# Optimization experiments

Hardware: AMD Instinct MI355X
Metric: run time of the kernel (lower is better)

Reference implementation:

```python
import jax, jax.numpy as jnp
import numpy as np

B, N, D, C = 2, 65536, 128, 128          # batch, n_entries, input_dim, channel_dim
DEG, N_ACTIVE, STRIDE = 16, 4096, 16     # ring-neighbor sparse structure


def _build_indices():
    """Replicates the original module's Python intersection loops exactly,
    flattening them into (src_i, src_j, pair_out) gather/scatter index arrays.
    k[:, e, :] = sum_m a[:, i_th[m], :] * b[:, j_th[m], :] for each write slot e.
    Each slot e is written exactly once, so scatter-add == the original set."""
    neigh = [[] for _ in range(N)]
    for t in range(N_ACTIVE):
        i = t * STRIDE
        neigh[i] = [((t + dlt) % N_ACTIVE) * STRIDE for dlt in range(1, DEG + 1)]
    src_i, src_j, out = [], [], []
    e = 0
    for i in range(N):
        if not neigh[i]:
            continue
        i_element = list(neigh[i]) + [i]
        i_set = set(i_element)
        for j in neigh[i]:
            j_list = neigh[j]
            j_set = set(j_list)
            j_th = [m for m in j_list if m in i_set]      # order of j's list
            i_th = [m for m in i_element if m in j_set]   # order of i_element
            for ai, bi in zip(i_th, j_th):
                src_i.append(ai)
                src_j.append(bi)
                out.append(e)
            e += 1
    return (np.asarray(src_i, np.int32), np.asarray(src_j, np.int32),
            np.asarray(out, np.int32))


def setup_inputs() -> dict:
    key = jax.random.key(0)
    ks = jax.random.split(key, 8)
    s = 1.0 / np.sqrt(D)
    src_i, src_j, pair_out = _build_indices()
    return {
        "x": jax.random.normal(ks[0], (B, N, D), jnp.float32),
        "ln_in_w": jnp.ones((D,), jnp.float32),
        "ln_in_b": jnp.zeros((D,), jnp.float32),
        "Wla": jax.random.normal(ks[1], (C, D), jnp.float32) * s,
        "bla": jnp.zeros((C,), jnp.float32),
        "Wga": jax.random.normal(ks[2], (C, D), jnp.float32) * s,
        "bga": jnp.zeros((C,), jnp.float32),
        "Wlb": jax.random.normal(ks[3], (C, D), jnp.float32) * s,
        "blb": jnp.zeros((C,), jnp.float32),
        "Wgb": jax.random.normal(ks[4], (C, D), jnp.float32) * s,
        "bgb": jnp.zeros((C,), jnp.float32),
        "ln_o_w": jnp.ones((C,), jnp.float32),
        "ln_o_b": jnp.zeros((C,), jnp.float32),
        "Wgo": jax.random.normal(ks[5], (D, D), jnp.float32) * s,
        "bgo": jnp.zeros((D,), jnp.float32),
        "Wlo": jax.random.normal(ks[6], (D, C), jnp.float32) * s,
        "blo": jnp.zeros((D,), jnp.float32),
        "src_i": jnp.asarray(src_i),
        "src_j": jnp.asarray(src_j),
        "pair_out": jnp.asarray(pair_out),
    }


def _layernorm(x, w, b, eps=1e-5):
    mu = jnp.mean(x, axis=-1, keepdims=True)
    var = jnp.mean(jnp.square(x - mu), axis=-1, keepdims=True)
    return (x - mu) * jax.lax.rsqrt(var + eps) * w + b


def reference(x, ln_in_w, ln_in_b, Wla, bla, Wga, bga, Wlb, blb, Wgb, bgb,
              ln_o_w, ln_o_b, Wgo, bgo, Wlo, blo, src_i, src_j, pair_out):
    xn = _layernorm(x, ln_in_w, ln_in_b)                              # [B,N,D]
    a = jax.nn.sigmoid(xn @ Wga.T + bga) * (xn @ Wla.T + bla)         # [B,N,C]
    b = jax.nn.sigmoid(xn @ Wgb.T + bgb) * (xn @ Wlb.T + blb)         # [B,N,C]
    # triangular update: gather-multiply-sum-scatter over precomputed pairs
    prod = a[:, src_i, :] * b[:, src_j, :]                            # [B,P,C]
    k = jnp.zeros_like(a).at[:, pair_out, :].add(prod)                # [B,N,C]
    out = jax.nn.sigmoid(xn @ Wgo.T + bgo) * (_layernorm(k, ln_o_w, ln_o_b) @ Wlo.T + blo)
    return out
```

## Files before the change

kernel.cpp:

```cpp
#include <hip/hip_runtime.h>


#define BB 2
#define NN 65536
#define DD 128
#define CC 128
#define NA 4096
#define STR 16
#define WSZ 16384

typedef short short4v __attribute__((ext_vector_type(4)));
typedef short short8v __attribute__((ext_vector_type(8)));
typedef __bf16 bf16x8 __attribute__((ext_vector_type(8)));
typedef float f32x4 __attribute__((ext_vector_type(4)));
typedef float f32x2 __attribute__((ext_vector_type(2)));

__device__ __forceinline__ float sigf(float v) { return 1.0f / (1.0f + __expf(-v)); }
__device__ __forceinline__ short nbf(float f) {
    union { __bf16 h; short s; } u; u.h = (__bf16)f; return u.s;
}
__device__ __forceinline__ float bf2f(short b) {
    union { unsigned u; float f; } v; v.u = ((unsigned)(unsigned short)b) << 16;
    return v.f;
}
__device__ __forceinline__ bf16x8 s2b(short8v s) {
    union { short8v s; bf16x8 b; } u; u.s = s; return u.b;
}

__global__ __launch_bounds__(256)
void kern_wcvt(const float* __restrict__ Wla, const float* __restrict__ Wga,
               const float* __restrict__ Wlb, const float* __restrict__ Wgb,
               const float* __restrict__ Wgo, const float* __restrict__ Wlo,
               const float* __restrict__ lnw, const float* __restrict__ lnb,
               const float* __restrict__ lnow, const float* __restrict__ lnob,
               const float* __restrict__ bla, const float* __restrict__ bga,
               const float* __restrict__ blb, const float* __restrict__ bgb,
               const float* __restrict__ bgo, const float* __restrict__ blo,
               short* __restrict__ wbf, float* __restrict__ vtab)
{
    const int b = blockIdx.x;
    if (b < 64) {
        const int i  = b * 256 + threadIdx.x;
        const int ch = i >> 7, d = i & 127;
        const int pos = ((ch >> 4) * 4 + (d >> 5)) * 512
                      + ((((d >> 3) & 3) * 16 + (ch & 15)) * 8) + (d & 7);
        const float wi = lnw[d], wo = lnow[d];
        wbf[pos]           = nbf(Wla[i] * wi);
        wbf[WSZ + pos]     = nbf(Wga[i] * wi);
        wbf[2 * WSZ + pos] = nbf(Wlb[i] * wi);
        wbf[3 * WSZ + pos] = nbf(Wgb[i] * wi);
        wbf[4 * WSZ + pos] = nbf(Wgo[i] * wi);
        wbf[5 * WSZ + pos] = nbf(Wlo[i] * wo);
    } else {
        const int t = (b - 64) * 256 + threadIdx.x;
        const int m = t >> 7, c = t & 127;
        const float* Wr = (m == 0) ? Wla : (m == 1) ? Wga : (m == 2) ? Wlb
                        : (m == 3) ? Wgb : (m == 4) ? Wgo : Wlo;
        const float* bb = (m == 5) ? lnob : lnb;
        const float* ww = (m == 5) ? lnow : lnw;
        const float* bi = (m == 0) ? bla : (m == 1) ? bga : (m == 2) ? blb
                        : (m == 3) ? bgb : (m == 4) ? bgo : blo;
        const float* row = Wr + (size_t)c * DD;
        float av = 0.f, as = 0.f;
        for (int d = 0; d < DD; d += 4) {
            const f32x4 w4 = *(const f32x4*)(row + d);
            const f32x4 b4 = *(const f32x4*)(bb + d);
            const f32x4 g4 = *(const f32x4*)(ww + d);
            av += w4[0]*b4[0] + w4[1]*b4[1] + w4[2]*b4[2] + w4[3]*b4[3];
            as += w4[0]*g4[0] + w4[1]*g4[1] + w4[2]*g4[2] + w4[3]*g4[3];
        }
        vtab[m * 128 + c]       = av + bi[c];
        vtab[768 + m * 128 + c] = as;
    }
}

__global__ __launch_bounds__(256)
void kern_ab(const float* __restrict__ x, const short* __restrict__ wbf,
             const float* __restrict__ vtab, float* __restrict__ cbuf)
{
    const int wv    = threadIdx.x >> 6;
    const int l     = threadIdx.x & 63;
    const int bid   = blockIdx.x * 4 + wv;
    const int batch = bid >> 9;
    const int t0    = ((bid & 511) >> 1) << 4;
    const int nt0   = (bid & 1) * 4;
    const int lr    = l & 15;
    const int q     = l >> 4;
    const int fl    = l * 8;

    const float* xr = x + ((size_t)batch * NN + (size_t)(t0 + lr) * STR) * DD + q * 8;
    f32x4 v[4][2];
    #pragma unroll
    for (int kk = 0; kk < 4; ++kk) {
        v[kk][0] = *(const f32x4*)(xr + kk * 32);
        v[kk][1] = *(const f32x4*)(xr + kk * 32 + 4);
    }
    float s = 0.f, ss = 0.f;
    #pragma unroll
    for (int kk = 0; kk < 4; ++kk)
        #pragma unroll
        for (int h = 0; h < 2; ++h)
            #pragma unroll
            for (int j = 0; j < 4; ++j) { const float f = v[kk][h][j]; s += f; ss += f * f; }
    s += __shfl_xor(s, 16); ss += __shfl_xor(ss, 16);
    s += __shfl_xor(s, 32); ss += __shfl_xor(ss, 32);
    const float mu = s * (1.0f / 128.0f);
    const float rs = rsqrtf(ss * (1.0f / 128.0f) - mu * mu + 1e-5f);
    const float p  = -mu * rs;

    bf16x8 af[4];
    #pragma unroll
    for (int kk = 0; kk < 4; ++kk) {
        short8v t;
        #pragma unroll
        for (int j = 0; j < 4; ++j) {
            t[j]     = nbf(v[kk][0][j] * rs + p);
            t[4 + j] = nbf(v[kk][1][j] * rs + p);
        }
        af[kk] = s2b(t);
    }

    const short* wla = wbf;
    const short* wga = wbf + WSZ;
    const short* wlb = wbf + 2 * WSZ;
    const short* wgb = wbf + 3 * WSZ;

    #pragma unroll
    for (int nt = 0; nt < 4; ++nt) {
        const int col  = (nt0 + nt) * 16 + lr;
        const int base = ((nt0 + nt) * 4) * 512 + fl;
        f32x4 ala = {0.f,0.f,0.f,0.f}, aga = {0.f,0.f,0.f,0.f};
        f32x4 alb = {0.f,0.f,0.f,0.f}, agb = {0.f,0.f,0.f,0.f};
        #pragma unroll
        for (int kk = 0; kk < 4; ++kk) {
            const int o = base + kk * 512;
            ala = __builtin_amdgcn_mfma_f32_16x16x32_bf16(af[kk], *(const bf16x8*)(wla + o), ala, 0, 0, 0);
            aga = __builtin_amdgcn_mfma_f32_16x16x32_bf16(af[kk], *(const bf16x8*)(wga + o), aga, 0, 0, 0);
            alb = __builtin_amdgcn_mfma_f32_16x16x32_bf16(af[kk], *(const bf16x8*)(wlb + o), alb, 0, 0, 0);
            agb = __builtin_amdgcn_mfma_f32_16x16x32_bf16(af[kk], *(const bf16x8*)(wgb + o), agb, 0, 0, 0);
        }
        const float vla = vtab[col], vga = vtab[128 + col];
        const float vlb = vtab[256 + col], vgb = vtab[384 + col];
        #pragma unroll
        for (int r = 0; r < 4; ++r) {
            const float av = sigf(aga[r] + vga) * (ala[r] + vla);
            const float bv = sigf(agb[r] + vgb) * (alb[r] + vlb);
            cbuf[((size_t)batch * NA + t0 + q * 4 + r) * CC + col] = av * bv;
        }
    }
}

__global__ __launch_bounds__(64)
void kern_out(const float* __restrict__ x, const short* __restrict__ wbf,
              const float* __restrict__ vtab, const float* __restrict__ cbuf,
              float* __restrict__ out)
{
    __shared__ short kls[2][16][136];
    __shared__ float kst[2][16][2];
    const int bid   = blockIdx.x;
    const int swz   = (bid & 7) * 512 + (bid >> 3);
    const int batch = swz >> 11;
    const int ib    = swz & 2047;
    const int row0  = ib * 32;
    const int t0    = ib * 2;

    const int l  = threadIdx.x;
    const int lr = l & 15, lk = l >> 4;
    const int fl = l * 8;

    f32x4 v[2][4][2];
    #pragma unroll
    for (int g = 0; g < 2; ++g) {
        const float* xr = x + ((size_t)batch * NN + row0 + g * 16 + lr) * DD + lk * 8;
        #pragma unroll
        for (int kk = 0; kk < 4; ++kk) {
            v[g][kk][0] = *(const f32x4*)(xr + kk * 32);
            v[g][kk][1] = *(const f32x4*)(xr + kk * 32 + 4);
        }
    }

    const int sg = l >> 5;
    const int c4 = (l & 31) * 4;
    const int t  = t0 + sg;
    f32x4 cv[15];
    #pragma unroll
    for (int sx = 14; sx >= 0; --sx)
        cv[sx] = *(const f32x4*)(cbuf + ((size_t)batch * NA + ((t + sx + 2) & (NA - 1))) * CC + c4);

    {
        short4v z = {0, 0, 0, 0};
        *(short4v*)&kls[sg][15][c4] = z;
        float s0 = 0.f, s1 = 0.f, s2 = 0.f, s3 = 0.f;
        #pragma unroll
        for (int sx = 14; sx >= 0; --sx) {
            s0 += cv[sx][0]; s1 += cv[sx][1]; s2 += cv[sx][2]; s3 += cv[sx][3];
            short4v o; o[0] = nbf(s0); o[1] = nbf(s1); o[2] = nbf(s2); o[3] = nbf(s3);
            *(short4v*)&kls[sg][sx][c4] = o;
        }
    }

    bf16x8 afx[2][4];
    #pragma unroll
    for (int g = 0; g < 2; ++g) {
        float s = 0.f, ss = 0.f;
        #pragma unroll
        for (int kk = 0; kk < 4; ++kk)
            #pragma unroll
            for (int h = 0; h < 2; ++h)
                #pragma unroll
                for (int j = 0; j < 4; ++j) { const float f = v[g][kk][h][j]; s += f; ss += f * f; }
        s += __shfl_xor(s, 16); ss += __shfl_xor(ss, 16);
        s += __shfl_xor(s, 32); ss += __shfl_xor(ss, 32);
        const float mu = s * (1.0f / 128.0f);
        const float rs = rsqrtf(ss * (1.0f / 128.0f) - mu * mu + 1e-5f);
        const float p  = -mu * rs;
        #pragma unroll
        for (int kk = 0; kk < 4; ++kk) {
            short8v o;
            #pragma unroll
            for (int j = 0; j < 4; ++j) {
                o[j]     = nbf(v[g][kk][0][j] * rs + p);
                o[4 + j] = nbf(v[g][kk][1][j] * rs + p);
            }
            afx[g][kk] = s2b(o);
        }
    }

    bf16x8 afk[2][4];
    short8v kraw[2][4];
    #pragma unroll
    for (int g = 0; g < 2; ++g)
        #pragma unroll
        for (int kk = 0; kk < 4; ++kk) {
            kraw[g][kk] = *(const short8v*)&kls[g][lr][kk * 32 + lk * 8];
            afk[g][kk]  = s2b(kraw[g][kk]);
        }

    #pragma unroll
    for (int g = 0; g < 2; ++g) {
        float ks = 0.f, kss = 0.f;
        #pragma unroll
        for (int kk = 0; kk < 4; ++kk)
            #pragma unroll
            for (int j = 0; j < 8; ++j) { const float f = bf2f(kraw[g][kk][j]); ks += f; kss += f * f; }
        ks += __shfl_xor(ks, 16); kss += __shfl_xor(kss, 16);
        ks += __shfl_xor(ks, 32); kss += __shfl_xor(kss, 32);
        const float kmu = ks * (1.0f / 128.0f);
        const float krs = rsqrtf(kss * (1.0f / 128.0f) - kmu * kmu + 1e-5f);
        if (lk == 0) { kst[g][lr][0] = krs; kst[g][lr][1] = -kmu * krs; }
    }
    f32x2 kp[2][4];
    #pragma unroll
    for (int g = 0; g < 2; ++g)
        #pragma unroll
        for (int r = 0; r < 4; ++r)
            kp[g][r] = *(const f32x2*)&kst[g][lk * 4 + r][0];

    const short* wgo = wbf + 4 * WSZ;
    const short* wlo = wbf + 5 * WSZ;
    const float* vgo = vtab + 4 * 128;
    const float* vlo = vtab + 5 * 128;
    const float* slo = vtab + 768 + 5 * 128;
    #pragma unroll
    for (int nt = 0; nt < 8; ++nt) {
        bf16x8 bg_[4], bh_[4];
        #pragma unroll
        for (int kk = 0; kk < 4; ++kk) {
            bg_[kk] = *(const bf16x8*)(wgo + (nt * 4 + kk) * 512 + fl);
            bh_[kk] = *(const bf16x8*)(wlo + (nt * 4 + kk) * 512 + fl);
        }
        f32x4 ag0 = {0.f,0.f,0.f,0.f}, ag1 = {0.f,0.f,0.f,0.f};
        f32x4 ah0 = {0.f,0.f,0.f,0.f}, ah1 = {0.f,0.f,0.f,0.f};
        #pragma unroll
        for (int kk = 0; kk < 4; ++kk) {
            ag0 = __builtin_amdgcn_mfma_f32_16x16x32_bf16(afx[0][kk], bg_[kk], ag0, 0, 0, 0);
            ag1 = __builtin_amdgcn_mfma_f32_16x16x32_bf16(afx[1][kk], bg_[kk], ag1, 0, 0, 0);
            ah0 = __builtin_amdgcn_mfma_f32_16x16x32_bf16(afk[0][kk], bh_[kk], ah0, 0, 0, 0);
            ah1 = __builtin_amdgcn_mfma_f32_16x16x32_bf16(afk[1][kk], bh_[kk], ah1, 0, 0, 0);
        }
        const int   col = nt * 16 + lr;
        const float vg  = vgo[col];
        const float vl  = vlo[col];
        const float sl  = slo[col];
        #pragma unroll
        for (int r = 0; r < 4; ++r) {
            const size_t rowa = (size_t)batch * NN + row0 + lk * 4 + r;
            const float h0 = kp[0][r][0] * ah0[r] + (kp[0][r][1] * sl + vl);
            const float h1 = kp[1][r][0] * ah1[r] + (kp[1][r][1] * sl + vl);
            out[rowa * DD + col]        = sigf(ag0[r] + vg) * h0;
            out[(rowa + 16) * DD + col] = sigf(ag1[r] + vg) * h1;
        }
    }
}

extern "C" void kernel_launch(void* const* d_in, const int* in_sizes, int n_in,
                              void* d_out, int out_size, void* d_ws, size_t ws_size,
                              hipStream_t stream)
{
    const float* x    = (const float*)d_in[0];
    const float* lnw  = (const float*)d_in[1];
    const float* lnb  = (const float*)d_in[2];
    const float* Wla  = (const float*)d_in[3];
    const float* bla  = (const float*)d_in[4];
    const float* Wga  = (const float*)d_in[5];
    const float* bga  = (const float*)d_in[6];
    const float* Wlb  = (const float*)d_in[7];
    const float* blb  = (const float*)d_in[8];
    const float* Wgb  = (const float*)d_in[9];
    const float* bgb  = (const float*)d_in[10];
    const float* lnow = (const float*)d_in[11];
    const float* lnob = (const float*)d_in[12];
    const float* Wgo  = (const float*)d_in[13];
    const float* bgo  = (const float*)d_in[14];
    const float* Wlo  = (const float*)d_in[15];
    const float* blo  = (const float*)d_in[16];

    float* cbuf = (float*)d_ws;
    short* wbf  = (short*)((char*)d_ws + (size_t)BB * NA * CC * 4);
    float* vtab = (float*)((char*)wbf + 6 * WSZ * sizeof(short));
    float* out  = (float*)d_out;

    hipLaunchKernelGGL(kern_wcvt, dim3(67), dim3(256), 0, stream,
                       Wla, Wga, Wlb, Wgb, Wgo, Wlo,
                       lnw, lnb, lnow, lnob,
                       bla, bga, blb, bgb, bgo, blo, wbf, vtab);
    hipLaunchKernelGGL(kern_ab, dim3(BB * 128), dim3(256), 0, stream,
                       x, wbf, vtab, cbuf);
    hipLaunchKernelGGL(kern_out, dim3(BB * 2048), dim3(64), 0, stream,
                       x, wbf, vtab, cbuf, out);
}
```

Measured before the change: 56.67 us.

## Switch output projection to 32x32x16 MFMA with matching weight layout

Rewrites the output kernel to use 32x32x16 bf16 MFMA instead of pairs of 16x16x32 MFMAs. The Wgo/Wlo weights are repacked into a 32-column tile layout, and the x and k fragments are reloaded in the matching lane mapping. This reduces the number of MFMA issues and per-tile weight loads. The cost is a new 16-row output scatter pattern and larger accumulator register use.

After: 59.46 us. 4.9% more time.

```diff
diff --git a/kernel.cpp b/kernel.cpp
--- a/kernel.cpp
+++ b/kernel.cpp
@@ -14,6 +14,7 @@
 typedef __bf16 bf16x8 __attribute__((ext_vector_type(8)));
 typedef float f32x4 __attribute__((ext_vector_type(4)));
 typedef float f32x2 __attribute__((ext_vector_type(2)));
+typedef float f32x16 __attribute__((ext_vector_type(16)));
 
 __device__ __forceinline__ float sigf(float v) { return 1.0f / (1.0f + __expf(-v)); }
 __device__ __forceinline__ short nbf(float f) {
@@ -42,15 +43,17 @@
     if (b < 64) {
         const int i  = b * 256 + threadIdx.x;
         const int ch = i >> 7, d = i & 127;
-        const int pos = ((ch >> 4) * 4 + (d >> 5)) * 512
-                      + ((((d >> 3) & 3) * 16 + (ch & 15)) * 8) + (d & 7);
+        const int pos16 = ((ch >> 4) * 4 + (d >> 5)) * 512
+                        + ((((d >> 3) & 3) * 16 + (ch & 15)) * 8) + (d & 7);
+        const int pos32 = ((ch >> 5) * 8 + (d >> 4)) * 512
+                        + ((((d >> 3) & 1) * 32 + (ch & 31)) * 8) + (d & 7);
         const float wi = lnw[d], wo = lnow[d];
-        wbf[pos]           = nbf(Wla[i] * wi);
-        wbf[WSZ + pos]     = nbf(Wga[i] * wi);
-        wbf[2 * WSZ + pos] = nbf(Wlb[i] * wi);
-        wbf[3 * WSZ + pos] = nbf(Wgb[i] * wi);
-        wbf[4 * WSZ + pos] = nbf(Wgo[i] * wi);
-        wbf[5 * WSZ + pos] = nbf(Wlo[i] * wo);
+        wbf[pos16]           = nbf(Wla[i] * wi);
+        wbf[WSZ + pos16]     = nbf(Wga[i] * wi);
+        wbf[2 * WSZ + pos16] = nbf(Wlb[i] * wi);
+        wbf[3 * WSZ + pos16] = nbf(Wgb[i] * wi);
+        wbf[4 * WSZ + pos32] = nbf(Wgo[i] * wi);
+        wbf[5 * WSZ + pos32] = nbf(Wlo[i] * wo);
     } else {
         const int t = (b - 64) * 256 + threadIdx.x;
         const int m = t >> 7, c = t & 127;
@@ -156,7 +159,7 @@
               float* __restrict__ out)
 {
     __shared__ short kls[2][16][136];
-    __shared__ float kst[2][16][2];
+    __shared__ float kst[32][2];
     const int bid   = blockIdx.x;
     const int swz   = (bid & 7) * 512 + (bid >> 3);
     const int batch = swz >> 11;
@@ -164,24 +167,13 @@
     const int row0  = ib * 32;
     const int t0    = ib * 2;
 
-    const int l  = threadIdx.x;
-    const int lr = l & 15, lk = l >> 4;
-    const int fl = l * 8;
-
-    f32x4 v[2][4][2];
-    #pragma unroll
-    for (int g = 0; g < 2; ++g) {
-        const float* xr = x + ((size_t)batch * NN + row0 + g * 16 + lr) * DD + lk * 8;
-        #pragma unroll
-        for (int kk = 0; kk < 4; ++kk) {
-            v[g][kk][0] = *(const f32x4*)(xr + kk * 32);
-            v[g][kk][1] = *(const f32x4*)(xr + kk * 32 + 4);
-        }
-    }
-
-    const int sg = l >> 5;
-    const int c4 = (l & 31) * 4;
-    const int t  = t0 + sg;
+    const int l   = threadIdx.x;
+    const int idx = l & 31;
+    const int q   = l >> 5;
+    const int fl  = l * 8;
+
+    const int c4 = idx * 4;
+    const int t  = t0 + q;
     f32x4 cv[15];
     #pragma unroll
     for (int sx = 14; sx >= 0; --sx)
@@ -189,72 +181,70 @@
 
     {
         short4v z = {0, 0, 0, 0};
-        *(short4v*)&kls[sg][15][c4] = z;
+        *(short4v*)&kls[q][15][c4] = z;
         float s0 = 0.f, s1 = 0.f, s2 = 0.f, s3 = 0.f;
         #pragma unroll
         for (int sx = 14; sx >= 0; --sx) {
             s0 += cv[sx][0]; s1 += cv[sx][1]; s2 += cv[sx][2]; s3 += cv[sx][3];
             short4v o; o[0] = nbf(s0); o[1] = nbf(s1); o[2] = nbf(s2); o[3] = nbf(s3);
-            *(short4v*)&kls[sg][sx][c4] = o;
-        }
-    }
-
-    bf16x8 afx[2][4];
-    #pragma unroll
-    for (int g = 0; g < 2; ++g) {
+            *(short4v*)&kls[q][sx][c4] = o;
+        }
+    }
+
+    const float* xr = x + ((size_t)batch * NN + row0 + idx) * DD + q * 8;
+    f32x4 xv[8][2];
+    #pragma unroll
+    for (int kb = 0; kb < 8; ++kb) {
+        xv[kb][0] = *(const f32x4*)(xr + kb * 16);
+        xv[kb][1] = *(const f32x4*)(xr + kb * 16 + 4);
+    }
+
+    const int gi = idx >> 4, ri = idx & 15;
+    short8v kr[8];
+    #pragma unroll
+    for (int kb = 0; kb < 8; ++kb)
+        kr[kb] = *(const short8v*)&kls[gi][ri][kb * 16 + q * 8];
+
+    {
+        float ks = 0.f, kss = 0.f;
+        #pragma unroll
+        for (int kb = 0; kb < 8; ++kb)
+            #pragma unroll
+            for (int j = 0; j < 8; ++j) { const float f = bf2f(kr[kb][j]); ks += f; kss += f * f; }
+        ks += __shfl_xor(ks, 32); kss += __shfl_xor(kss, 32);
+        const float kmu = ks * (1.0f / 128.0f);
+        const float krs = rsqrtf(kss * (1.0f / 128.0f) - kmu * kmu + 1e-5f);
+        if (q == 0) { kst[idx][0] = krs; kst[idx][1] = -kmu * krs; }
+    }
+    f32x2 kpr[16];
+    #pragma unroll
+    for (int r = 0; r < 16; ++r)
+        kpr[r] = *(const f32x2*)&kst[(r & 3) + 8 * (r >> 2) + 4 * q][0];
+
+    bf16x8 afx[8];
+    {
         float s = 0.f, ss = 0.f;
         #pragma unroll
-        for (int kk = 0; kk < 4; ++kk)
+        for (int kb = 0; kb < 8; ++kb)
             #pragma unroll
             for (int h = 0; h < 2; ++h)
                 #pragma unroll
-                for (int j = 0; j < 4; ++j) { const float f = v[g][kk][h][j]; s += f; ss += f * f; }
-        s += __shfl_xor(s, 16); ss += __shfl_xor(ss, 16);
+                for (int j = 0; j < 4; ++j) { const float f = xv[kb][h][j]; s += f; ss += f * f; }
         s += __shfl_xor(s, 32); ss += __shfl_xor(ss, 32);
         const float mu = s * (1.0f / 128.0f);
         const float rs = rsqrtf(ss * (1.0f / 128.0f) - mu * mu + 1e-5f);
         const float p  = -mu * rs;
         #pragma unroll
-        for (int kk = 0; kk < 4; ++kk) {
+        for (int kb = 0; kb < 8; ++kb) {
             short8v o;
             #pragma unroll
             for (int j = 0; j < 4; ++j) {
-                o[j]     = nbf(v[g][kk][0][j] * rs + p);
-                o[4 + j] = nbf(v[g][kk][1][j] * rs + p);
+                o[j]     = nbf(xv[kb][0][j] * rs + p);
+                o[4 + j] = nbf(xv[kb][1][j] * rs + p);
             }
-            afx[g][kk] = s2b(o);
-        }
-    }
-
-    bf16x8 afk[2][4];
-    short8v kraw[2][4];
-    #pragma unroll
-    for (int g = 0; g < 2; ++g)
-        #pragma unroll
-        for (int kk = 0; kk < 4; ++kk) {
-            kraw[g][kk] = *(const short8v*)&kls[g][lr][kk * 32 + lk * 8];
-            afk[g][kk]  = s2b(kraw[g][kk]);
-        }
-
-    #pragma unroll
-    for (int g = 0; g < 2; ++g) {
-        float ks = 0.f, kss = 0.f;
-        #pragma unroll
-        for (int kk = 0; kk < 4; ++kk)
-            #pragma unroll
-            for (int j = 0; j < 8; ++j) { const float f = bf2f(kraw[g][kk][j]); ks += f; kss += f * f; }
-        ks += __shfl_xor(ks, 16); kss += __shfl_xor(kss, 16);
-        ks += __shfl_xor(ks, 32); kss += __shfl_xor(kss, 32);
-        const float kmu = ks * (1.0f / 128.0f);
-        const float krs = rsqrtf(kss * (1.0f / 128.0f) - kmu * kmu + 1e-5f);
-        if (lk == 0) { kst[g][lr][0] = krs; kst[g][lr][1] = -kmu * krs; }
-    }
-    f32x2 kp[2][4];
-    #pragma unroll
-    for (int g = 0; g < 2; ++g)
-        #pragma unroll
-        for (int r = 0; r < 4; ++r)
-            kp[g][r] = *(const f32x2*)&kst[g][lk * 4 + r][0];
+            afx[kb] = s2b(o);
+        }
+    }
 
     const short* wgo = wbf + 4 * WSZ;
     const short* wlo = wbf + 5 * WSZ;
@@ -262,33 +252,26 @@
     const float* vlo = vtab + 5 * 128;
     const float* slo = vtab + 768 + 5 * 128;
     #pragma unroll
-    for (int nt = 0; nt < 8; ++nt) {
-        bf16x8 bg_[4], bh_[4];
-        #pragma unroll
-        for (int kk = 0; kk < 4; ++kk) {
-            bg_[kk] = *(const bf16x8*)(wgo + (nt * 4 + kk) * 512 + fl);
-            bh_[kk] = *(const bf16x8*)(wlo + (nt * 4 + kk) * 512 + fl);
-        }
-        f32x4 ag0 = {0.f,0.f,0.f,0.f}, ag1 = {0.f,0.f,0.f,0.f};
-        f32x4 ah0 = {0.f,0.f,0.f,0.f}, ah1 = {0.f,0.f,0.f,0.f};
-        #pragma unroll
-        for (int kk = 0; kk < 4; ++kk) {
-            ag0 = __builtin_amdgcn_mfma_f32_16x16x32_bf16(afx[0][kk], bg_[kk], ag0, 0, 0, 0);
-            ag1 = __builtin_amdgcn_mfma_f32_16x16x32_bf16(afx[1][kk], bg_[kk], ag1, 0, 0, 0);
-            ah0 = __builtin_amdgcn_mfma_f32_16x16x32_bf16(afk[0][kk], bh_[kk], ah0, 0, 0, 0);
-            ah1 = __builtin_amdgcn_mfma_f32_16x16x32_bf16(afk[1][kk], bh_[kk], ah1, 0, 0, 0);
-        }
-        const int   col = nt * 16 + lr;
+    for (int nt = 0; nt < 4; ++nt) {
+        f32x16 ag, ah;
+        #pragma unroll
+        for (int i = 0; i < 16; ++i) { ag[i] = 0.f; ah[i] = 0.f; }
+        #pragma unroll
+        for (int kb = 0; kb < 8; ++kb) {
+            const int o = (nt * 8 + kb) * 512 + fl;
+            ag = __builtin_amdgcn_mfma_f32_32x32x16_bf16(afx[kb], *(const bf16x8*)(wgo + o), ag, 0, 0, 0);
+            ah = __builtin_amdgcn_mfma_f32_32x32x16_bf16(s2b(kr[kb]), *(const bf16x8*)(wlo + o), ah, 0, 0, 0);
+        }
+        const int   col = nt * 32 + idx;
         const float vg  = vgo[col];
         const float vl  = vlo[col];
         const float sl  = slo[col];
         #pragma unroll
-        for (int r = 0; r < 4; ++r) {
-            const size_t rowa = (size_t)batch * NN + row0 + lk * 4 + r;
-            const float h0 = kp[0][r][0] * ah0[r] + (kp[0][r][1] * sl + vl);
-            const float h1 = kp[1][r][0] * ah1[r] + (kp[1][r][1] * sl + vl);
-            out[rowa * DD + col]        = sigf(ag0[r] + vg) * h0;
-            out[(rowa + 16) * DD + col] = sigf(ag1[r] + vg) * h1;
+        for (int r = 0; r < 16; ++r) {
+            const int crow = (r & 3) + 8 * (r >> 2) + 4 * q;
+            const size_t rowa = (size_t)batch * NN + row0 + crow;
+            const float h = kpr[r][0] * ah[r] + (kpr[r][1] * sl + vl);
+            out[rowa * DD + col] = sigf(ag[r] + vg) * h;
         }
     }
 }
```

## Split output kernel into gate and k-projection waves with 64-row tiles

Applied to the files above, without the earlier changes.

The output kernel now runs two waves per block over 64 rows instead of one wave over 32. Wave 0 layer-norms x, computes the sigmoid gate GEMM and stages the gates as bf16 in shared memory. Wave 1 first builds the k prefix sums from cbuf, then after a barrier applies the k layernorm, the Wlo GEMM and the gating. The operands are swapped so each lane writes contiguous f32x4 outputs, which should give more weight reuse and wider stores. The cost is a block barrier, a serialized gate-then-output dependency between the waves, extra shared memory, and gates rounded to bf16.

After: 64.73 us. 1.14x slower.

```diff
diff --git a/kernel.cpp b/kernel.cpp
--- a/kernel.cpp
+++ b/kernel.cpp
@@ -13,7 +13,6 @@
 typedef short short8v __attribute__((ext_vector_type(8)));
 typedef __bf16 bf16x8 __attribute__((ext_vector_type(8)));
 typedef float f32x4 __attribute__((ext_vector_type(4)));
-typedef float f32x2 __attribute__((ext_vector_type(2)));
 
 __device__ __forceinline__ float sigf(float v) { return 1.0f / (1.0f + __expf(-v)); }
 __device__ __forceinline__ short nbf(float f) {
@@ -150,145 +149,158 @@
     }
 }
 
-__global__ __launch_bounds__(64)
+__global__ __launch_bounds__(128)
 void kern_out(const float* __restrict__ x, const short* __restrict__ wbf,
               const float* __restrict__ vtab, const float* __restrict__ cbuf,
               float* __restrict__ out)
 {
-    __shared__ short kls[2][16][136];
-    __shared__ float kst[2][16][2];
+    __shared__ short kls[4][16][136];
+    __shared__ short gls[64][136];
     const int bid   = blockIdx.x;
-    const int swz   = (bid & 7) * 512 + (bid >> 3);
-    const int batch = swz >> 11;
-    const int ib    = swz & 2047;
-    const int row0  = ib * 32;
-    const int t0    = ib * 2;
-
-    const int l  = threadIdx.x;
+    const int swz   = (bid & 7) * 256 + (bid >> 3);
+    const int batch = swz >> 10;
+    const int ib    = swz & 1023;
+    const int row0  = ib * 64;
+    const int t0    = ib * 4;
+
+    const int wave = threadIdx.x >> 6;
+    const int l    = threadIdx.x & 63;
     const int lr = l & 15, lk = l >> 4;
     const int fl = l * 8;
 
-    f32x4 v[2][4][2];
-    #pragma unroll
-    for (int g = 0; g < 2; ++g) {
-        const float* xr = x + ((size_t)batch * NN + row0 + g * 16 + lr) * DD + lk * 8;
-        #pragma unroll
-        for (int kk = 0; kk < 4; ++kk) {
-            v[g][kk][0] = *(const f32x4*)(xr + kk * 32);
-            v[g][kk][1] = *(const f32x4*)(xr + kk * 32 + 4);
-        }
-    }
-
-    const int sg = l >> 5;
-    const int c4 = (l & 31) * 4;
-    const int t  = t0 + sg;
-    f32x4 cv[15];
-    #pragma unroll
-    for (int sx = 14; sx >= 0; --sx)
-        cv[sx] = *(const f32x4*)(cbuf + ((size_t)batch * NA + ((t + sx + 2) & (NA - 1))) * CC + c4);
-
-    {
-        short4v z = {0, 0, 0, 0};
-        *(short4v*)&kls[sg][15][c4] = z;
-        float s0 = 0.f, s1 = 0.f, s2 = 0.f, s3 = 0.f;
-        #pragma unroll
-        for (int sx = 14; sx >= 0; --sx) {
-            s0 += cv[sx][0]; s1 += cv[sx][1]; s2 += cv[sx][2]; s3 += cv[sx][3];
-            short4v o; o[0] = nbf(s0); o[1] = nbf(s1); o[2] = nbf(s2); o[3] = nbf(s3);
-            *(short4v*)&kls[sg][sx][c4] = o;
-        }
-    }
-
-    bf16x8 afx[2][4];
-    #pragma unroll
-    for (int g = 0; g < 2; ++g) {
-        float s = 0.f, ss = 0.f;
-        #pragma unroll
-        for (int kk = 0; kk < 4; ++kk)
-            #pragma unroll
-            for (int h = 0; h < 2; ++h)
-                #pragma unroll
-                for (int j = 0; j < 4; ++j) { const float f = v[g][kk][h][j]; s += f; ss += f * f; }
-        s += __shfl_xor(s, 16); ss += __shfl_xor(ss, 16);
-        s += __shfl_xor(s, 32); ss += __shfl_xor(ss, 32);
-        const float mu = s * (1.0f / 128.0f);
-        const float rs = rsqrtf(ss * (1.0f / 128.0f) - mu * mu + 1e-5f);
-        const float p  = -mu * rs;
-        #pragma unroll
-        for (int kk = 0; kk < 4; ++kk) {
-            short8v o;
-            #pragma unroll
-            for (int j = 0; j < 4; ++j) {
-                o[j]     = nbf(v[g][kk][0][j] * rs + p);
-                o[4 + j] = nbf(v[g][kk][1][j] * rs + p);
-            }
-            afx[g][kk] = s2b(o);
-        }
-    }
-
-    bf16x8 afk[2][4];
-    short8v kraw[2][4];
-    #pragma unroll
-    for (int g = 0; g < 2; ++g)
-        #pragma unroll
-        for (int kk = 0; kk < 4; ++kk) {
-            kraw[g][kk] = *(const short8v*)&kls[g][lr][kk * 32 + lk * 8];
-            afk[g][kk]  = s2b(kraw[g][kk]);
-        }
-
-    #pragma unroll
-    for (int g = 0; g < 2; ++g) {
-        float ks = 0.f, kss = 0.f;
-        #pragma unroll
-        for (int kk = 0; kk < 4; ++kk)
-            #pragma unroll
-            for (int j = 0; j < 8; ++j) { const float f = bf2f(kraw[g][kk][j]); ks += f; kss += f * f; }
-        ks += __shfl_xor(ks, 16); kss += __shfl_xor(kss, 16);
-        ks += __shfl_xor(ks, 32); kss += __shfl_xor(kss, 32);
-        const float kmu = ks * (1.0f / 128.0f);
-        const float krs = rsqrtf(kss * (1.0f / 128.0f) - kmu * kmu + 1e-5f);
-        if (lk == 0) { kst[g][lr][0] = krs; kst[g][lr][1] = -kmu * krs; }
-    }
-    f32x2 kp[2][4];
-    #pragma unroll
-    for (int g = 0; g < 2; ++g)
-        #pragma unroll
-        for (int r = 0; r < 4; ++r)
-            kp[g][r] = *(const f32x2*)&kst[g][lk * 4 + r][0];
-
-    const short* wgo = wbf + 4 * WSZ;
-    const short* wlo = wbf + 5 * WSZ;
-    const float* vgo = vtab + 4 * 128;
-    const float* vlo = vtab + 5 * 128;
-    const float* slo = vtab + 768 + 5 * 128;
-    #pragma unroll
-    for (int nt = 0; nt < 8; ++nt) {
-        bf16x8 bg_[4], bh_[4];
-        #pragma unroll
-        for (int kk = 0; kk < 4; ++kk) {
-            bg_[kk] = *(const bf16x8*)(wgo + (nt * 4 + kk) * 512 + fl);
-            bh_[kk] = *(const bf16x8*)(wlo + (nt * 4 + kk) * 512 + fl);
-        }
-        f32x4 ag0 = {0.f,0.f,0.f,0.f}, ag1 = {0.f,0.f,0.f,0.f};
-        f32x4 ah0 = {0.f,0.f,0.f,0.f}, ah1 = {0.f,0.f,0.f,0.f};
-        #pragma unroll
-        for (int kk = 0; kk < 4; ++kk) {
-            ag0 = __builtin_amdgcn_mfma_f32_16x16x32_bf16(afx[0][kk], bg_[kk], ag0, 0, 0, 0);
-            ag1 = __builtin_amdgcn_mfma_f32_16x16x32_bf16(afx[1][kk], bg_[kk], ag1, 0, 0, 0);
-            ah0 = __builtin_amdgcn_mfma_f32_16x16x32_bf16(afk[0][kk], bh_[kk], ah0, 0, 0, 0);
-            ah1 = __builtin_amdgcn_mfma_f32_16x16x32_bf16(afk[1][kk], bh_[kk], ah1, 0, 0, 0);
-        }
-        const int   col = nt * 16 + lr;
-        const float vg  = vgo[col];
-        const float vl  = vlo[col];
-        const float sl  = slo[col];
-        #pragma unroll
-        for (int r = 0; r < 4; ++r) {
-            const size_t rowa = (size_t)batch * NN + row0 + lk * 4 + r;
-            const float h0 = kp[0][r][0] * ah0[r] + (kp[0][r][1] * sl + vl);
-            const float h1 = kp[1][r][0] * ah1[r] + (kp[1][r][1] * sl + vl);
-            out[rowa * DD + col]        = sigf(ag0[r] + vg) * h0;
-            out[(rowa + 16) * DD + col] = sigf(ag1[r] + vg) * h1;
+    if (wave == 0) {
+        bf16x8 xf[4][4];
+        #pragma unroll
+        for (int rt = 0; rt < 4; ++rt) {
+            const float* xr = x + ((size_t)batch * NN + row0 + rt * 16 + lr) * DD + lk * 8;
+            f32x4 v[4][2];
+            #pragma unroll
+            for (int kk = 0; kk < 4; ++kk) {
+                v[kk][0] = *(const f32x4*)(xr + kk * 32);
+                v[kk][1] = *(const f32x4*)(xr + kk * 32 + 4);
+            }
+            float s = 0.f, ss = 0.f;
+            #pragma unroll
+            for (int kk = 0; kk < 4; ++kk)
+                #pragma unroll
+                for (int h = 0; h < 2; ++h)
+                    #pragma unroll
+                    for (int j = 0; j < 4; ++j) { const float f = v[kk][h][j]; s += f; ss += f * f; }
+            s += __shfl_xor(s, 16); ss += __shfl_xor(ss, 16);
+            s += __shfl_xor(s, 32); ss += __shfl_xor(ss, 32);
+            const float mu = s * (1.0f / 128.0f);
+            const float rs = rsqrtf(ss * (1.0f / 128.0f) - mu * mu + 1e-5f);
+            const float p  = -mu * rs;
+            #pragma unroll
+            for (int kk = 0; kk < 4; ++kk) {
+                short8v o;
+                #pragma unroll
+                for (int j = 0; j < 4; ++j) {
+                    o[j]     = nbf(v[kk][0][j] * rs + p);
+                    o[4 + j] = nbf(v[kk][1][j] * rs + p);
+                }
+                xf[rt][kk] = s2b(o);
+            }
+        }
+        const short* wgo = wbf + 4 * WSZ;
+        const float* vgo = vtab + 4 * 128;
+        #pragma unroll
+        for (int nt = 0; nt < 8; ++nt) {
+            f32x4 acc[4];
+            #pragma unroll
+            for (int rt = 0; rt < 4; ++rt) acc[rt] = (f32x4){0.f, 0.f, 0.f, 0.f};
+            #pragma unroll
+            for (int kk = 0; kk < 4; ++kk) {
+                const bf16x8 wf = *(const bf16x8*)(wgo + (nt * 4 + kk) * 512 + fl);
+                #pragma unroll
+                for (int rt = 0; rt < 4; ++rt)
+                    acc[rt] = __builtin_amdgcn_mfma_f32_16x16x32_bf16(wf, xf[rt][kk], acc[rt], 0, 0, 0);
+            }
+            const f32x4 vg4 = *(const f32x4*)(vgo + nt * 16 + lk * 4);
+            #pragma unroll
+            for (int rt = 0; rt < 4; ++rt) {
+                short4v g;
+                #pragma unroll
+                for (int r = 0; r < 4; ++r) g[r] = nbf(sigf(acc[rt][r] + vg4[r]));
+                *(short4v*)&gls[rt * 16 + lr][nt * 16 + lk * 4] = g;
+            }
+        }
+    } else {
+        #pragma unroll
+        for (int p = 0; p < 2; ++p) {
+            const int g  = p * 2 + (l >> 5);
+            const int c4 = (l & 31) * 4;
+            const int t  = t0 + g;
+            f32x4 cv[15];
+            #pragma unroll
+            for (int sx = 14; sx >= 0; --sx)
+                cv[sx] = *(const f32x4*)(cbuf + ((size_t)batch * NA + ((t + sx + 2) & (NA - 1))) * CC + c4);
+            short4v z = {0, 0, 0, 0};
+            *(short4v*)&kls[g][15][c4] = z;
+            float s0 = 0.f, s1 = 0.f, s2 = 0.f, s3 = 0.f;
+            #pragma unroll
+            for (int sx = 14; sx >= 0; --sx) {
+                s0 += cv[sx][0]; s1 += cv[sx][1]; s2 += cv[sx][2]; s3 += cv[sx][3];
+                short4v o; o[0] = nbf(s0); o[1] = nbf(s1); o[2] = nbf(s2); o[3] = nbf(s3);
+                *(short4v*)&kls[g][sx][c4] = o;
+            }
+        }
+    }
+
+    __syncthreads();
+
+    if (wave == 1) {
+        bf16x8 kf[4][4];
+        float krs[4], kp[4];
+        #pragma unroll
+        for (int rt = 0; rt < 4; ++rt) {
+            short8v kraw[4];
+            #pragma unroll
+            for (int kk = 0; kk < 4; ++kk) {
+                kraw[kk] = *(const short8v*)&kls[rt][lr][kk * 32 + lk * 8];
+                kf[rt][kk] = s2b(kraw[kk]);
+            }
+            float ks = 0.f, kss = 0.f;
+            #pragma unroll
+            for (int kk = 0; kk < 4; ++kk)
+                #pragma unroll
+                for (int j = 0; j < 8; ++j) { const float f = bf2f(kraw[kk][j]); ks += f; kss += f * f; }
+            ks += __shfl_xor(ks, 16); kss += __shfl_xor(kss, 16);
+            ks += __shfl_xor(ks, 32); kss += __shfl_xor(kss, 32);
+            const float kmu = ks * (1.0f / 128.0f);
+            krs[rt] = rsqrtf(kss * (1.0f / 128.0f) - kmu * kmu + 1e-5f);
+            kp[rt]  = -kmu * krs[rt];
+        }
+
+        const short* wlo = wbf + 5 * WSZ;
+        const float* vlo = vtab + 5 * 128;
+        const float* slo = vtab + 768 + 5 * 128;
+        #pragma unroll
+        for (int nt = 0; nt < 8; ++nt) {
+            f32x4 acc[4];
+            #pragma unroll
+            for (int rt = 0; rt < 4; ++rt) acc[rt] = (f32x4){0.f, 0.f, 0.f, 0.f};
+            #pragma unroll
+            for (int kk = 0; kk < 4; ++kk) {
+                const bf16x8 wf = *(const bf16x8*)(wlo + (nt * 4 + kk) * 512 + fl);
+                #pragma unroll
+                for (int rt = 0; rt < 4; ++rt)
+                    acc[rt] = __builtin_amdgcn_mfma_f32_16x16x32_bf16(wf, kf[rt][kk], acc[rt], 0, 0, 0);
+            }
+            const f32x4 vl4 = *(const f32x4*)(vlo + nt * 16 + lk * 4);
+            const f32x4 sl4 = *(const f32x4*)(slo + nt * 16 + lk * 4);
+            #pragma unroll
+            for (int rt = 0; rt < 4; ++rt) {
+                const short4v g = *(const short4v*)&gls[rt * 16 + lr][nt * 16 + lk * 4];
+                f32x4 o;
+                #pragma unroll
+                for (int r = 0; r < 4; ++r) {
+                    const float h = krs[rt] * acc[rt][r] + (kp[rt] * sl4[r] + vl4[r]);
+                    o[r] = bf2f(g[r]) * h;
+                }
+                *(f32x4*)(out + ((size_t)batch * NN + row0 + rt * 16 + lr) * DD
+                              + nt * 16 + lk * 4) = o;
+            }
         }
     }
 }
@@ -326,6 +338,6 @@
                        bla, bga, blb, bgb, bgo, blo, wbf, vtab);
     hipLaunchKernelGGL(kern_ab, dim3(BB * 128), dim3(256), 0, stream,
                        x, wbf, vtab, cbuf);
-    hipLaunchKernelGGL(kern_out, dim3(BB * 2048), dim3(64), 0, stream,
+    hipLaunchKernelGGL(kern_out, dim3(BB * 1024), dim3(128), 0, stream,
                        x, wbf, vtab, cbuf, out);
 }
```
